# Optimization experiments

Hardware: AMD Instinct MI355X
Metric: run time of the kernel (lower is better)

Reference implementation:

```python
import jax, jax.numpy as jnp
import numpy as np

N = 50000       # nodes
E = 1600000     # edges (before self-loops)
H = 4           # heads
C = 32          # channels per head
G = 64          # graphs in batch
NEG_SLOPE = 0.2


def gat_conv(x, src, dst, W, att_src, att_dst, bias):
    # x: [N, Fin]; W: [Fin, H*C]; att_*: [H, C]; bias: [H*C]
    h = (x @ W).reshape(N, H, C)                       # [N, H, C]
    a_src = jnp.einsum('nhc,hc->nh', h, att_src)       # [N, H]
    a_dst = jnp.einsum('nhc,hc->nh', h, att_dst)       # [N, H]
    e = a_src[src] + a_dst[dst]                        # [E', H]
    e = jax.nn.leaky_relu(e, NEG_SLOPE)
    # softmax over incoming edges of each destination node
    m = jax.ops.segment_max(e, dst, num_segments=N)    # [N, H]
    ex = jnp.exp(e - m[dst])
    denom = jax.ops.segment_sum(ex, dst, num_segments=N)  # [N, H]
    alpha = ex / (denom[dst] + 1e-16)                  # [E', H]
    msg = h[src] * alpha[:, :, None]                   # [E', H, C]
    out = jax.ops.segment_sum(msg, dst, num_segments=N)  # [N, H, C]
    return out.reshape(N, H * C) + bias


def setup_inputs() -> dict:
    key = jax.random.key(0)
    ks = jax.random.split(key, 12)
    x = jax.random.normal(ks[0], (N, 128), dtype=jnp.float32)
    edge_index = jax.random.randint(ks[1], (2, E), 0, N, dtype=jnp.int64)
    batch = jnp.sort(jax.random.randint(ks[2], (N,), 0, G, dtype=jnp.int64))
    s = 0.05
    return {
        'x': x,
        'edge_index': edge_index,
        'batch': batch,
        'W1': jax.random.normal(ks[3], (128, H * C), dtype=jnp.float32) * s,
        'att_src1': jax.random.normal(ks[4], (H, C), dtype=jnp.float32) * s,
        'att_dst1': jax.random.normal(ks[5], (H, C), dtype=jnp.float32) * s,
        'b1': jnp.zeros((H * C,), dtype=jnp.float32),
        'W2': jax.random.normal(ks[6], (H * C, H * C), dtype=jnp.float32) * s,
        'att_src2': jax.random.normal(ks[7], (H, C), dtype=jnp.float32) * s,
        'att_dst2': jax.random.normal(ks[8], (H, C), dtype=jnp.float32) * s,
        'b2': jnp.zeros((H * C,), dtype=jnp.float32),
        'fc_W': jax.random.normal(ks[9], (H * C, 8), dtype=jnp.float32) * s,
        'fc_b': jnp.zeros((8,), dtype=jnp.float32),
    }


def reference(x, edge_index, batch, W1, att_src1, att_dst1, b1,
              W2, att_src2, att_dst2, b2, fc_W, fc_b):
    # add self loops (PyG GATConv default)
    ar = jnp.arange(N, dtype=edge_index.dtype)
    src = jnp.concatenate([edge_index[0], ar])
    dst = jnp.concatenate([edge_index[1], ar])
    h = gat_conv(x, src, dst, W1, att_src1, att_dst1, b1)
    h = jax.nn.elu(h)
    h = gat_conv(h, src, dst, W2, att_src2, att_dst2, b2)
    # global mean pool over graphs
    sums = jax.ops.segment_sum(h, batch, num_segments=G)          # [G, HC]
    cnt = jax.ops.segment_sum(jnp.ones((N,), h.dtype), batch, num_segments=G)
    pooled = sums / jnp.maximum(cnt, 1.0)[:, None]
    logits = pooled @ fc_W + fc_b                                  # [G, 8]
    return jax.nn.log_softmax(logits, axis=1)
```

## Files before the change

kernel.cpp:

```cpp
#include <hip/hip_runtime.h>
#include <math.h>

#define HC 128
#define GG 64
#define NEG 0.2f
#define TILE 8192
#define BW 128
#define SLOT 8192
#define NBMAX 512
#define LDA 136
#define PPARTS 8

typedef __attribute__((ext_vector_type(8))) short short8;
typedef __attribute__((ext_vector_type(4))) float floatx4;
typedef __attribute__((ext_vector_type(2))) float floatx2;

static __device__ __forceinline__ float leaky(float x) { return x > 0.f ? x : NEG * x; }

static __device__ __forceinline__ unsigned short f2bf(float f) {
    unsigned u = __float_as_uint(f);
    u += 0x7FFF + ((u >> 16) & 1);
    return (unsigned short)(u >> 16);
}
static __device__ __forceinline__ float bf2f(unsigned short s) {
    return __uint_as_float(((unsigned)s) << 16);
}

#if __has_builtin(__builtin_amdgcn_cvt_pk_f32_fp8) && __has_builtin(__builtin_amdgcn_cvt_pk_fp8_f32)
template <bool HI>
static __device__ __forceinline__ floatx2 fp8pair(unsigned int w) {
    return __builtin_amdgcn_cvt_pk_f32_fp8((int)w, HI);
}
static __device__ __forceinline__ unsigned int f32x2_fp8(float a, float b) {
    return ((unsigned int)__builtin_amdgcn_cvt_pk_fp8_f32(a, b, 0, false)) & 0xFFFFu;
}
#else
static __device__ __forceinline__ float fp8one(unsigned v) {
    unsigned e = (v >> 3) & 15u, m = v & 7u;
    float mag = e ? __uint_as_float(((e + 120u) << 23) | (m << 20))
                  : (float)m * 0.001953125f;
    return (v & 0x80u) ? -mag : mag;
}
template <bool HI>
static __device__ __forceinline__ floatx2 fp8pair(unsigned int w) {
    unsigned h = HI ? (w >> 16) : w;
    floatx2 r; r.x = fp8one(h & 0xFFu); r.y = fp8one((h >> 8) & 0xFFu);
    return r;
}
static __device__ __forceinline__ unsigned fp8enc(float f) {
    unsigned u = __float_as_uint(f);
    unsigned s = (u >> 24) & 0x80u;
    float a = fabsf(f);
    if (a >= 448.f) return s | 0x7Eu;
    if (a < 0.015625f) {
        unsigned m = (unsigned)(int)rintf(a * 512.f);
        return s | m;
    }
    u = __float_as_uint(a);
    u += 0xFFFFFu + ((u >> 20) & 1u);
    unsigned e8 = (u >> 23) - 120u;
    if (e8 >= 16u) return s | 0x7Eu;
    return s | (e8 << 3) | ((u >> 20) & 7u);
}
static __device__ __forceinline__ unsigned int f32x2_fp8(float a, float b) {
    return fp8enc(a) | (fp8enc(b) << 8);
}
#endif

static __device__ __forceinline__ void acc16(floatx2* acc, float w, const uint4& d) {
    floatx2 w2 = {w, w};
    acc[0] += w2 * fp8pair<false>(d.x);
    acc[1] += w2 * fp8pair<true>(d.x);
    acc[2] += w2 * fp8pair<false>(d.y);
    acc[3] += w2 * fp8pair<true>(d.y);
    acc[4] += w2 * fp8pair<false>(d.z);
    acc[5] += w2 * fp8pair<true>(d.z);
    acc[6] += w2 * fp8pair<false>(d.w);
    acc[7] += w2 * fp8pair<true>(d.w);
}

__global__ __launch_bounds__(256) void setup_k(const float* __restrict__ W1,
                                               const float* __restrict__ W2,
                                               unsigned short* __restrict__ Wt1,
                                               unsigned short* __restrict__ Wt2,
                                               int* __restrict__ gbcur,
                                               const int* __restrict__ batch,
                                               int* __restrict__ node_end,
                                               int* __restrict__ row_start,
                                               int NB, int Nn, int M) {
    int i = blockIdx.x * 256 + threadIdx.x;
    if (i < NB) gbcur[i] = i * SLOT;
    if (i == 0) row_start[Nn] = M;
    if (i < 32768) {
        const float* W = (i >> 14) ? W2 : W1;
        unsigned short* Wt = (i >> 14) ? Wt2 : Wt1;
        int d = i & 16383;
        int j = d & 7;
        int m = (d >> 3) & 15;
        int qf = d >> 7;
        int q = qf & 3;
        int f = qf >> 2;
        int kb = f & 3;
        int ct = f >> 2;
        int n = ct * 16 + m;
        int k = kb * 32 + q * 8 + j;
        Wt[d] = f2bf(W[k * 128 + n]);
    }
    if (i < Nn) {
        int b = batch[i];
        if (i == 0) {
            for (int g = 0; g < b; g++) node_end[g] = 0;
        }
        int bn = (i + 1 < Nn) ? batch[i + 1] : GG;
        for (int g = b; g < bn; g++) node_end[g] = i + 1;
    }
}

__global__ __launch_bounds__(256) void binscat_k(const int* __restrict__ ei,
                                                 int* __restrict__ gbcur,
                                                 unsigned int* __restrict__ staging,
                                                 int E, int M, int NB) {
    __shared__ unsigned int reorder[TILE];
    __shared__ int s_cnt[NBMAX], s_off[NBMAX], s_run[NBMAX];
    __shared__ int s_wsum[8];
    __shared__ int s_carry;
    const int tid = threadIdx.x;
    const int lane = tid & 63, wid = tid >> 6;
    const int tbase = blockIdx.x * TILE;
    const int tcnt = min(TILE, M - tbase);

    for (int i = tid; i < NB; i += 256) s_cnt[i] = 0;
    if (tid == 0) s_carry = 0;
    __syncthreads();

    for (int t = tid; t < tcnt; t += 256) {
        int i = tbase + t;
        int dst = (i < E) ? ei[E + i] : (i - E);
        atomicAdd(&s_cnt[dst >> 7], 1);
    }
    __syncthreads();

    for (int base = 0; base < NB; base += 256) {
        int i = base + tid;
        int v = (i < NB) ? s_cnt[i] : 0;
        int incl = v;
        #pragma unroll
        for (int off = 1; off < 64; off <<= 1) {
            int u = __shfl_up(incl, off);
            if (lane >= off) incl += u;
        }
        if (lane == 63) s_wsum[wid] = incl;
        __syncthreads();
        if (tid == 0) {
            int a = 0;
            for (int w = 0; w < 4; w++) { int tv = s_wsum[w]; s_wsum[w] = a; a += tv; }
            s_wsum[4] = a;
        }
        __syncthreads();
        int excl = s_carry + s_wsum[wid] + incl - v;
        if (i < NB) s_off[i] = excl;
        __syncthreads();
        if (tid == 0) s_carry += s_wsum[4];
        __syncthreads();
    }

    for (int b = tid; b < NB; b += 256)
        s_run[b] = atomicAdd(&gbcur[b], s_cnt[b]);
    for (int b = tid; b < NB; b += 256) s_cnt[b] = s_off[b];
    __syncthreads();

    for (int t = tid; t < tcnt; t += 256) {
        int i = tbase + t;
        int src, dst;
        if (i < E) { src = ei[i]; dst = ei[E + i]; }
        else       { src = dst = i - E; }
        unsigned int p = ((unsigned int)dst << 16) | (unsigned int)src;
        int r = atomicAdd(&s_cnt[dst >> 7], 1);
        reorder[r] = p;
    }
    __syncthreads();

    for (int t = tid; t < tcnt; t += 256) {
        unsigned int p = reorder[t];
        int b = p >> 23;
        staging[s_run[b] + (t - s_off[b])] = p;
    }
}

__global__ __launch_bounds__(256) void unbin_k(const unsigned int* __restrict__ staging,
                                               const int* __restrict__ gbcur,
                                               int* __restrict__ row_start,
                                               unsigned short* __restrict__ srcs, int Nn) {
    __shared__ int s_cnt[BW];
    __shared__ int s_cur[BW];
    __shared__ int s_w[4];
    int b = blockIdx.x, t = threadIdx.x;
    int sbase = b * SLOT;
    int cnt = gbcur[b] - sbase;

    int pacc = 0;
    for (int i = t; i < b; i += 256) pacc += gbcur[i] - i * SLOT;
    #pragma unroll
    for (int off = 1; off < 64; off <<= 1) pacc += __shfl_xor(pacc, off);
    if ((t & 63) == 0) s_w[t >> 6] = pacc;
    __syncthreads();
    int bb = s_w[0] + s_w[1] + s_w[2] + s_w[3];
    __syncthreads();

    int n0 = b * BW;
    if (t < BW) s_cnt[t] = 0;
    __syncthreads();
    for (int j = t; j < cnt; j += 256)
        atomicAdd(&s_cnt[(staging[sbase + j] >> 16) & (BW - 1)], 1);
    __syncthreads();
    int v = (t < BW) ? s_cnt[t] : 0;
    int incl = v;
    #pragma unroll
    for (int off = 1; off < 64; off <<= 1) {
        int u = __shfl_up(incl, off);
        if ((t & 63) >= off) incl += u;
    }
    if (t < BW && (t & 63) == 63) s_w[t >> 6] = incl;
    __syncthreads();
    int excl = incl - v + ((t >= 64 && t < BW) ? s_w[0] : 0);
    if (t < BW) {
        s_cur[t] = bb + excl;
        if (n0 + t < Nn) row_start[n0 + t] = bb + excl;
    }
    __syncthreads();
    for (int j = t; j < cnt; j += 256) {
        unsigned int p = staging[sbase + j];
        int ln = (int)(p >> 16) & (BW - 1);
        int r = atomicAdd(&s_cur[ln], 1);
        srcs[r] = (unsigned short)(p & 0xFFFFu);
    }
}

__global__ __launch_bounds__(128) void gemm_fused(const void* __restrict__ Xv,
                                                  int x_f32,
                                                  const unsigned short* __restrict__ Wt,
                                                  const float* __restrict__ att_s,
                                                  const float* __restrict__ att_d,
                                                  unsigned char* __restrict__ H8,
                                                  float* __restrict__ a_src,
                                                  float* __restrict__ a_dst,
                                                  int n_rows) {
    __shared__ unsigned short As[64 * LDA];
    const int tid = threadIdx.x;
    const int row0 = blockIdx.x * 64;

    if (x_f32) {
        const float* X = (const float*)Xv;
        for (int i = tid; i < 2048; i += 128) {
            int r = i >> 5;
            int c4 = (i & 31) << 2;
            int gr = row0 + r;
            float4 v = (gr < n_rows) ? ((const float4*)&X[(size_t)gr * 128])[i & 31]
                                     : make_float4(0.f, 0.f, 0.f, 0.f);
            ushort4 bv = {f2bf(v.x), f2bf(v.y), f2bf(v.z), f2bf(v.w)};
            *(ushort4*)&As[r * LDA + c4] = bv;
        }
    } else {
        const unsigned short* X = (const unsigned short*)Xv;
        for (int i = tid; i < 1024; i += 128) {
            int r = i >> 4;
            int c8 = (i & 15) << 3;
            int gr = row0 + r;
            uint4 v = (gr < n_rows) ? *(const uint4*)&X[(size_t)gr * 128 + c8]
                                    : make_uint4(0, 0, 0, 0);
            *(uint4*)&As[r * LDA + c8] = v;
        }
    }
    __syncthreads();

    const int lane = tid & 63;
    const int wave = tid >> 6;
    const int m = lane & 15;
    const int quad = lane >> 4;
    const int wr0 = wave * 32;

    floatx4 acc[2][8];
    #pragma unroll
    for (int nt = 0; nt < 2; nt++)
        #pragma unroll
        for (int ct = 0; ct < 8; ct++)
            acc[nt][ct] = (floatx4){0.f, 0.f, 0.f, 0.f};

    #pragma unroll
    for (int kb = 0; kb < 4; kb++) {
        short8 x0 = *(const short8*)&As[(wr0 + m) * LDA + kb * 32 + quad * 8];
        short8 x1 = *(const short8*)&As[(wr0 + 16 + m) * LDA + kb * 32 + quad * 8];
        #pragma unroll
        for (int ct = 0; ct < 8; ct++) {
            short8 wf = *(const short8*)&Wt[(((ct * 4 + kb) * 4) + quad) * 128 + m * 8];
            acc[0][ct] = __builtin_amdgcn_mfma_f32_16x16x32_bf16(wf, x0, acc[0][ct], 0, 0, 0);
            acc[1][ct] = __builtin_amdgcn_mfma_f32_16x16x32_bf16(wf, x1, acc[1][ct], 0, 0, 0);
        }
    }

    const int q4 = quad * 4;
    #pragma unroll
    for (int nt = 0; nt < 2; nt++) {
        int node = row0 + wr0 + nt * 16 + m;
        bool vld = node < n_rows;
        float ps[4] = {0.f, 0.f, 0.f, 0.f};
        float pd[4] = {0.f, 0.f, 0.f, 0.f};
        #pragma unroll
        for (int ct = 0; ct < 8; ct++) {
            floatx4 v = acc[nt][ct];
            int c0 = ct * 16 + q4;
            float4 avs = *(const float4*)&att_s[c0];
            float4 avd = *(const float4*)&att_d[c0];
            int h = ct >> 1;
            ps[h] += v[0] * avs.x + v[1] * avs.y + v[2] * avs.z + v[3] * avs.w;
            pd[h] += v[0] * avd.x + v[1] * avd.y + v[2] * avd.z + v[3] * avd.w;
            if (vld) {
                unsigned pk01 = f32x2_fp8(v[0], v[1]);
                unsigned pk23 = f32x2_fp8(v[2], v[3]);
                *(unsigned*)&H8[(size_t)node * 128 + c0] = pk01 | (pk23 << 16);
            }
        }
        #pragma unroll
        for (int h = 0; h < 4; h++) {
            ps[h] += __shfl_xor(ps[h], 16); ps[h] += __shfl_xor(ps[h], 32);
            pd[h] += __shfl_xor(pd[h], 16); pd[h] += __shfl_xor(pd[h], 32);
        }
        if (lane < 16 && vld) {
            float4 s4 = {ps[0], ps[1], ps[2], ps[3]};
            float4 d4 = {pd[0], pd[1], pd[2], pd[3]};
            *(float4*)&a_src[node * 4] = s4;
            *(float4*)&a_dst[node * 4] = d4;
        }
    }
}

__global__ __launch_bounds__(256) void gat_agg(const unsigned char* __restrict__ H8,
                                               const float* __restrict__ a_src,
                                               const float* __restrict__ a_dst,
                                               const int* __restrict__ row_start,
                                               const unsigned short* __restrict__ srcs,
                                               const float* __restrict__ bias,
                                               unsigned short* __restrict__ OUT,
                                               int n_rows, int elu) {
    int n = (blockIdx.x * 256 + threadIdx.x) >> 3;
    if (n >= n_rows) return;
    int li = threadIdx.x & 7;
    int hd = li >> 1;
    int base = row_start[n];
    int end = row_start[n + 1];
    float adh = a_dst[n * 4 + hd];

    floatx2 acc[8];
    #pragma unroll
    for (int k = 0; k < 8; k++) acc[k] = (floatx2){0.f, 0.f};
    float wsum = 0.f;

    int j = base;
    int head_n = min(end - j, (4 - (base & 3)) & 3);
    for (int q = 0; q < head_n; q++, j++) {
        int s0 = srcs[j];
        float w0 = __expf(leaky(a_src[s0 * 4 + hd] + adh));
        uint4 d0 = *(const uint4*)&H8[(size_t)s0 * 128 + li * 16];
        acc16(acc, w0, d0);
        wsum += w0;
    }
    for (; j + 4 <= end; j += 4) {
        uint2 sv = *(const uint2*)&srcs[j];
        int s0 = sv.x & 0xFFFFu, s1 = sv.x >> 16;
        int s2 = sv.y & 0xFFFFu, s3 = sv.y >> 16;
        float a0 = a_src[s0 * 4 + hd];
        float a1 = a_src[s1 * 4 + hd];
        float a2 = a_src[s2 * 4 + hd];
        float a3 = a_src[s3 * 4 + hd];
        uint4 d0 = *(const uint4*)&H8[(size_t)s0 * 128 + li * 16];
        uint4 d1 = *(const uint4*)&H8[(size_t)s1 * 128 + li * 16];
        uint4 d2 = *(const uint4*)&H8[(size_t)s2 * 128 + li * 16];
        uint4 d3 = *(const uint4*)&H8[(size_t)s3 * 128 + li * 16];
        float w0 = __expf(leaky(a0 + adh));
        float w1 = __expf(leaky(a1 + adh));
        float w2 = __expf(leaky(a2 + adh));
        float w3 = __expf(leaky(a3 + adh));
        acc16(acc, w0, d0);
        acc16(acc, w1, d1);
        acc16(acc, w2, d2);
        acc16(acc, w3, d3);
        wsum += (w0 + w1) + (w2 + w3);
    }
    for (; j < end; j++) {
        int s0 = srcs[j];
        float w0 = __expf(leaky(a_src[s0 * 4 + hd] + adh));
        uint4 d0 = *(const uint4*)&H8[(size_t)s0 * 128 + li * 16];
        acc16(acc, w0, d0);
        wsum += w0;
    }

    float ih = 1.0f / (wsum + 1e-16f);
    float o[16];
    #pragma unroll
    for (int k = 0; k < 8; k++) {
        float2 bv = *(const float2*)&bias[li * 16 + 2 * k];
        o[2 * k]     = acc[k].x * ih + bv.x;
        o[2 * k + 1] = acc[k].y * ih + bv.y;
    }
    if (elu) {
        #pragma unroll
        for (int k = 0; k < 16; k++) o[k] = o[k] > 0.f ? o[k] : __expf(o[k]) - 1.f;
    }
    unsigned int pk[8];
    #pragma unroll
    for (int k = 0; k < 8; k++)
        pk[k] = ((unsigned)f2bf(o[2 * k + 1]) << 16) | (unsigned)f2bf(o[2 * k]);
    uint4 s0v = {pk[0], pk[1], pk[2], pk[3]};
    uint4 s1v = {pk[4], pk[5], pk[6], pk[7]};
    unsigned short* op = &OUT[(size_t)n * 128 + li * 16];
    *(uint4*)op = s0v;
    *(uint4*)(op + 8) = s1v;
}

__global__ __launch_bounds__(256) void pool_k(const unsigned* __restrict__ H2u,
                                              const int* __restrict__ node_end,
                                              float* __restrict__ partial) {
    __shared__ float ls[4][128];
    int g = blockIdx.x >> 3;
    int p = blockIdx.x & (PPARTS - 1);
    int s = (g > 0) ? node_end[g - 1] : 0;
    int e = node_end[g];
    int cnt = e - s;
    int chunk = (cnt + PPARTS - 1) >> 3;
    int n0 = s + p * chunk;
    int n1 = min(n0 + chunk, e);
    int col = threadIdx.x & 63;
    int nr = threadIdx.x >> 6;
    float ax = 0.f, ay = 0.f;
    for (int n = n0 + nr; n < n1; n += 4) {
        unsigned u = H2u[(size_t)n * 64 + col];
        ax += bf2f((unsigned short)(u & 0xFFFFu));
        ay += bf2f((unsigned short)(u >> 16));
    }
    ls[nr][col * 2] = ax;
    ls[nr][col * 2 + 1] = ay;
    __syncthreads();
    if (threadIdx.x < 128) {
        float v = ls[0][threadIdx.x] + ls[1][threadIdx.x] +
                  ls[2][threadIdx.x] + ls[3][threadIdx.x];
        partial[(size_t)(p * GG + g) * 128 + threadIdx.x] = v;
    }
}

__global__ __launch_bounds__(64) void head_k(const float* __restrict__ partial,
                                             const int* __restrict__ node_end,
                                             const float* __restrict__ fcW,
                                             const float* __restrict__ fcb,
                                             float* __restrict__ out) {
    __shared__ float p[128];
    __shared__ float lg[8];
    int g = blockIdx.x, t = threadIdx.x;
    int c = node_end[g] - (g > 0 ? node_end[g - 1] : 0);
    float cnt = fmaxf((float)c, 1.0f);
    float v0 = 0.f, v1 = 0.f;
    #pragma unroll
    for (int q = 0; q < PPARTS; q++) {
        v0 += partial[(size_t)(q * GG + g) * 128 + t];
        v1 += partial[(size_t)(q * GG + g) * 128 + 64 + t];
    }
    p[t] = v0 / cnt;
    p[t + 64] = v1 / cnt;
    __syncthreads();
    if (t < 8) {
        float s = fcb[t];
        for (int k = 0; k < 128; k++) s += p[k] * fcW[k * 8 + t];
        lg[t] = s;
    }
    __syncthreads();
    if (t == 0) {
        float m = lg[0];
        for (int j = 1; j < 8; j++) m = fmaxf(m, lg[j]);
        float se = 0.f;
        for (int j = 0; j < 8; j++) se += expf(lg[j] - m);
        float lse = logf(se) + m;
        for (int j = 0; j < 8; j++) out[g * 8 + j] = lg[j] - lse;
    }
}

extern "C" void kernel_launch(void* const* d_in, const int* in_sizes, int n_in,
                              void* d_out, int out_size, void* d_ws, size_t ws_size,
                              hipStream_t stream) {
    const float* x    = (const float*)d_in[0];
    const int*   ei   = (const int*)d_in[1];
    const int*   batch= (const int*)d_in[2];
    const float* W1   = (const float*)d_in[3];
    const float* as1  = (const float*)d_in[4];
    const float* ad1  = (const float*)d_in[5];
    const float* b1   = (const float*)d_in[6];
    const float* W2   = (const float*)d_in[7];
    const float* as2  = (const float*)d_in[8];
    const float* ad2  = (const float*)d_in[9];
    const float* b2   = (const float*)d_in[10];
    const float* fcW  = (const float*)d_in[11];
    const float* fcb  = (const float*)d_in[12];
    float* out = (float*)d_out;

    const int Nn = in_sizes[0] / HC;
    const int E  = in_sizes[1] / 2;
    const int M  = E + Nn;
    const int NB = (Nn + BW - 1) / BW;

    char* ws = (char*)d_ws;
    size_t off = 0;
    auto alloc = [&](size_t bytes) -> char* {
        char* p = ws + off;
        off = (off + bytes + 255) & ~(size_t)255;
        return p;
    };
    size_t hB_bytes  = (size_t)Nn * HC * 2;
    size_t stg_bytes = (size_t)NB * SLOT * 4;
    char* hB_region = alloc(hB_bytes > stg_bytes ? hB_bytes : stg_bytes);
    unsigned short* hB      = (unsigned short*)hB_region;
    unsigned int*   staging = (unsigned int*)hB_region;
    unsigned char*  H8      = (unsigned char*)alloc((size_t)Nn * HC);
    float* asrc      = (float*)alloc((size_t)Nn * 4 * 4);
    float* adst      = (float*)alloc((size_t)Nn * 4 * 4);
    unsigned short* srcs = (unsigned short*)alloc((size_t)M * 2);
    int*   row_start = (int*)alloc((size_t)(Nn + 1) * 4);
    float* partial   = (float*)alloc((size_t)PPARTS * GG * HC * 4);
    int*   node_end  = (int*)alloc((size_t)GG * 4);
    int*   gbcur     = (int*)alloc((size_t)NB * 4);
    unsigned short* Wt1 = (unsigned short*)alloc(16384 * 2);
    unsigned short* Wt2 = (unsigned short*)alloc(16384 * 2);

    setup_k<<<(Nn + 255) / 256, 256, 0, stream>>>(W1, W2, Wt1, Wt2, gbcur, batch,
                                                  node_end, row_start, NB, Nn, M);
    binscat_k<<<(M + TILE - 1) / TILE, 256, 0, stream>>>(ei, gbcur, staging, E, M, NB);
    unbin_k<<<NB, 256, 0, stream>>>(staging, gbcur, row_start, srcs, Nn);
    gemm_fused<<<(Nn + 63) / 64, 128, 0, stream>>>(x, 1, Wt1, as1, ad1, H8, asrc, adst, Nn);
    gat_agg<<<(Nn + 31) / 32, 256, 0, stream>>>(H8, asrc, adst, row_start, srcs, b1, hB, Nn, 1);
    gemm_fused<<<(Nn + 63) / 64, 128, 0, stream>>>(hB, 0, Wt2, as2, ad2, H8, asrc, adst, Nn);
    gat_agg<<<(Nn + 31) / 32, 256, 0, stream>>>(H8, asrc, adst, row_start, srcs, b2, hB, Nn, 0);
    pool_k<<<GG * PPARTS, 256, 0, stream>>>((const unsigned*)hB, node_end, partial);
    head_k<<<GG, 64, 0, stream>>>(partial, node_end, fcW, fcb, out);
}
```

Measured before the change: 262.5 us.

## Merge edge binning with layer-1 GEMM and fuse mean pooling into aggregation

Edge binning and the first-layer GEMM now run in one launch, with blocks split by index between the two roles, so the independent GEMM overlaps the binning work. The second aggregation writes per-block, per-graph partial sums straight from shared memory instead of writing hB and running a separate pooling kernel. The head kernel sums those block partials for each graph. This removes two launches and one full pass over the layer-2 output. The pooling assumes each 32-node block covers at most 4 graphs (it relies on sorted batch), and the layer-1 GEMM now uses 16 rows per wave.

```diff
diff --git a/kernel.cpp b/kernel.cpp
--- a/kernel.cpp
+++ b/kernel.cpp
@@ -9,7 +9,6 @@
 #define SLOT 8192
 #define NBMAX 512
 #define LDA 136
-#define PPARTS 8
 
 typedef __attribute__((ext_vector_type(8))) short short8;
 typedef __attribute__((ext_vector_type(4))) float floatx4;
@@ -116,74 +115,155 @@
     }
 }
 
-__global__ __launch_bounds__(256) void binscat_k(const int* __restrict__ ei,
-                                                 int* __restrict__ gbcur,
-                                                 unsigned int* __restrict__ staging,
-                                                 int E, int M, int NB) {
-    __shared__ unsigned int reorder[TILE];
-    __shared__ int s_cnt[NBMAX], s_off[NBMAX], s_run[NBMAX];
-    __shared__ int s_wsum[8];
-    __shared__ int s_carry;
+__global__ __launch_bounds__(256) void fused_k(const int* __restrict__ ei,
+                                               int* __restrict__ gbcur,
+                                               unsigned int* __restrict__ staging,
+                                               int E, int M, int NB, int NBIN,
+                                               const float* __restrict__ X,
+                                               const unsigned short* __restrict__ Wt,
+                                               const float* __restrict__ att_s,
+                                               const float* __restrict__ att_d,
+                                               unsigned char* __restrict__ H8,
+                                               float* __restrict__ a_src,
+                                               float* __restrict__ a_dst,
+                                               int n_rows) {
+    __shared__ __align__(16) char smem[39040];
     const int tid = threadIdx.x;
-    const int lane = tid & 63, wid = tid >> 6;
-    const int tbase = blockIdx.x * TILE;
-    const int tcnt = min(TILE, M - tbase);
-
-    for (int i = tid; i < NB; i += 256) s_cnt[i] = 0;
-    if (tid == 0) s_carry = 0;
-    __syncthreads();
-
-    for (int t = tid; t < tcnt; t += 256) {
-        int i = tbase + t;
-        int dst = (i < E) ? ei[E + i] : (i - E);
-        atomicAdd(&s_cnt[dst >> 7], 1);
-    }
-    __syncthreads();
-
-    for (int base = 0; base < NB; base += 256) {
-        int i = base + tid;
-        int v = (i < NB) ? s_cnt[i] : 0;
-        int incl = v;
-        #pragma unroll
-        for (int off = 1; off < 64; off <<= 1) {
-            int u = __shfl_up(incl, off);
-            if (lane >= off) incl += u;
-        }
-        if (lane == 63) s_wsum[wid] = incl;
+
+    if ((int)blockIdx.x < NBIN) {
+        unsigned int* reorder = (unsigned int*)smem;
+        int* s_cnt  = (int*)(smem + 32768);
+        int* s_off  = (int*)(smem + 34816);
+        int* s_run  = (int*)(smem + 36864);
+        int* s_wsum = (int*)(smem + 38912);
+        int* s_carry= (int*)(smem + 38944);
+        const int lane = tid & 63, wid = tid >> 6;
+        const int tbase = blockIdx.x * TILE;
+        const int tcnt = min(TILE, M - tbase);
+
+        for (int i = tid; i < NB; i += 256) s_cnt[i] = 0;
+        if (tid == 0) *s_carry = 0;
         __syncthreads();
-        if (tid == 0) {
-            int a = 0;
-            for (int w = 0; w < 4; w++) { int tv = s_wsum[w]; s_wsum[w] = a; a += tv; }
-            s_wsum[4] = a;
+
+        for (int t = tid; t < tcnt; t += 256) {
+            int i = tbase + t;
+            int dst = (i < E) ? ei[E + i] : (i - E);
+            atomicAdd(&s_cnt[dst >> 7], 1);
         }
         __syncthreads();
-        int excl = s_carry + s_wsum[wid] + incl - v;
-        if (i < NB) s_off[i] = excl;
+
+        for (int base = 0; base < NB; base += 256) {
+            int i = base + tid;
+            int v = (i < NB) ? s_cnt[i] : 0;
+            int incl = v;
+            #pragma unroll
+            for (int off = 1; off < 64; off <<= 1) {
+                int u = __shfl_up(incl, off);
+                if (lane >= off) incl += u;
+            }
+            if (lane == 63) s_wsum[wid] = incl;
+            __syncthreads();
+            if (tid == 0) {
+                int a = 0;
+                for (int w = 0; w < 4; w++) { int tv = s_wsum[w]; s_wsum[w] = a; a += tv; }
+                s_wsum[4] = a;
+            }
+            __syncthreads();
+            int excl = *s_carry + s_wsum[wid] + incl - v;
+            if (i < NB) s_off[i] = excl;
+            __syncthreads();
+            if (tid == 0) *s_carry += s_wsum[4];
+            __syncthreads();
+        }
+
+        for (int b = tid; b < NB; b += 256)
+            s_run[b] = atomicAdd(&gbcur[b], s_cnt[b]);
+        for (int b = tid; b < NB; b += 256) s_cnt[b] = s_off[b];
         __syncthreads();
-        if (tid == 0) s_carry += s_wsum[4];
+
+        for (int t = tid; t < tcnt; t += 256) {
+            int i = tbase + t;
+            int src, dst;
+            if (i < E) { src = ei[i]; dst = ei[E + i]; }
+            else       { src = dst = i - E; }
+            unsigned int p = ((unsigned int)dst << 16) | (unsigned int)src;
+            int r = atomicAdd(&s_cnt[dst >> 7], 1);
+            reorder[r] = p;
+        }
         __syncthreads();
-    }
-
-    for (int b = tid; b < NB; b += 256)
-        s_run[b] = atomicAdd(&gbcur[b], s_cnt[b]);
-    for (int b = tid; b < NB; b += 256) s_cnt[b] = s_off[b];
-    __syncthreads();
-
-    for (int t = tid; t < tcnt; t += 256) {
-        int i = tbase + t;
-        int src, dst;
-        if (i < E) { src = ei[i]; dst = ei[E + i]; }
-        else       { src = dst = i - E; }
-        unsigned int p = ((unsigned int)dst << 16) | (unsigned int)src;
-        int r = atomicAdd(&s_cnt[dst >> 7], 1);
-        reorder[r] = p;
-    }
-    __syncthreads();
-
-    for (int t = tid; t < tcnt; t += 256) {
-        unsigned int p = reorder[t];
-        int b = p >> 23;
-        staging[s_run[b] + (t - s_off[b])] = p;
+
+        for (int t = tid; t < tcnt; t += 256) {
+            unsigned int p = reorder[t];
+            int b = p >> 23;
+            staging[s_run[b] + (t - s_off[b])] = p;
+        }
+    } else {
+        unsigned short* As = (unsigned short*)smem;
+        const int gb = blockIdx.x - NBIN;
+        const int row0 = gb * 64;
+
+        for (int i = tid; i < 2048; i += 256) {
+            int r = i >> 5;
+            int c4 = (i & 31) << 2;
+            int gr = row0 + r;
+            float4 v = (gr < n_rows) ? ((const float4*)&X[(size_t)gr * 128])[i & 31]
+                                     : make_float4(0.f, 0.f, 0.f, 0.f);
+            ushort4 bv = {f2bf(v.x), f2bf(v.y), f2bf(v.z), f2bf(v.w)};
+            *(ushort4*)&As[r * LDA + c4] = bv;
+        }
+        __syncthreads();
+
+        const int lane = tid & 63;
+        const int wave = tid >> 6;
+        const int m = lane & 15;
+        const int quad = lane >> 4;
+        const int wr = wave * 16;
+
+        floatx4 acc[8];
+        #pragma unroll
+        for (int ct = 0; ct < 8; ct++) acc[ct] = (floatx4){0.f, 0.f, 0.f, 0.f};
+
+        #pragma unroll
+        for (int kb = 0; kb < 4; kb++) {
+            short8 x0 = *(const short8*)&As[(wr + m) * LDA + kb * 32 + quad * 8];
+            #pragma unroll
+            for (int ct = 0; ct < 8; ct++) {
+                short8 wf = *(const short8*)&Wt[(((ct * 4 + kb) * 4) + quad) * 128 + m * 8];
+                acc[ct] = __builtin_amdgcn_mfma_f32_16x16x32_bf16(wf, x0, acc[ct], 0, 0, 0);
+            }
+        }
+
+        const int q4 = quad * 4;
+        int node = row0 + wr + m;
+        bool vld = node < n_rows;
+        float ps[4] = {0.f, 0.f, 0.f, 0.f};
+        float pd[4] = {0.f, 0.f, 0.f, 0.f};
+        #pragma unroll
+        for (int ct = 0; ct < 8; ct++) {
+            floatx4 v = acc[ct];
+            int c0 = ct * 16 + q4;
+            float4 avs = *(const float4*)&att_s[c0];
+            float4 avd = *(const float4*)&att_d[c0];
+            int h = ct >> 1;
+            ps[h] += v[0] * avs.x + v[1] * avs.y + v[2] * avs.z + v[3] * avs.w;
+            pd[h] += v[0] * avd.x + v[1] * avd.y + v[2] * avd.z + v[3] * avd.w;
+            if (vld) {
+                unsigned pk01 = f32x2_fp8(v[0], v[1]);
+                unsigned pk23 = f32x2_fp8(v[2], v[3]);
+                *(unsigned*)&H8[(size_t)node * 128 + c0] = pk01 | (pk23 << 16);
+            }
+        }
+        #pragma unroll
+        for (int h = 0; h < 4; h++) {
+            ps[h] += __shfl_xor(ps[h], 16); ps[h] += __shfl_xor(ps[h], 32);
+            pd[h] += __shfl_xor(pd[h], 16); pd[h] += __shfl_xor(pd[h], 32);
+        }
+        if (lane < 16 && vld) {
+            float4 s4 = {ps[0], ps[1], ps[2], ps[3]};
+            float4 d4 = {pd[0], pd[1], pd[2], pd[3]};
+            *(float4*)&a_src[node * 4] = s4;
+            *(float4*)&a_dst[node * 4] = d4;
+        }
     }
 }
 
@@ -236,8 +316,7 @@
     }
 }
 
-__global__ __launch_bounds__(128) void gemm_fused(const void* __restrict__ Xv,
-                                                  int x_f32,
+__global__ __launch_bounds__(128) void gemm_fused(const unsigned short* __restrict__ X,
                                                   const unsigned short* __restrict__ Wt,
                                                   const float* __restrict__ att_s,
                                                   const float* __restrict__ att_d,
@@ -249,27 +328,13 @@
     const int tid = threadIdx.x;
     const int row0 = blockIdx.x * 64;
 
-    if (x_f32) {
-        const float* X = (const float*)Xv;
-        for (int i = tid; i < 2048; i += 128) {
-            int r = i >> 5;
-            int c4 = (i & 31) << 2;
-            int gr = row0 + r;
-            float4 v = (gr < n_rows) ? ((const float4*)&X[(size_t)gr * 128])[i & 31]
-                                     : make_float4(0.f, 0.f, 0.f, 0.f);
-            ushort4 bv = {f2bf(v.x), f2bf(v.y), f2bf(v.z), f2bf(v.w)};
-            *(ushort4*)&As[r * LDA + c4] = bv;
-        }
-    } else {
-        const unsigned short* X = (const unsigned short*)Xv;
-        for (int i = tid; i < 1024; i += 128) {
-            int r = i >> 4;
-            int c8 = (i & 15) << 3;
-            int gr = row0 + r;
-            uint4 v = (gr < n_rows) ? *(const uint4*)&X[(size_t)gr * 128 + c8]
-                                    : make_uint4(0, 0, 0, 0);
-            *(uint4*)&As[r * LDA + c8] = v;
-        }
+    for (int i = tid; i < 1024; i += 128) {
+        int r = i >> 4;
+        int c8 = (i & 15) << 3;
+        int gr = row0 + r;
+        uint4 v = (gr < n_rows) ? *(const uint4*)&X[(size_t)gr * 128 + c8]
+                                : make_uint4(0, 0, 0, 0);
+        *(uint4*)&As[r * LDA + c8] = v;
     }
     __syncthreads();
 
@@ -341,135 +406,154 @@
                                                const unsigned short* __restrict__ srcs,
                                                const float* __restrict__ bias,
                                                unsigned short* __restrict__ OUT,
-                                               int n_rows, int elu) {
+                                               const int* __restrict__ batch,
+                                               float* __restrict__ partial,
+                                               int n_rows, int mode) {
+    __shared__ float ls[32][128];
+    __shared__ int sg[32];
     int n = (blockIdx.x * 256 + threadIdx.x) >> 3;
-    if (n >= n_rows) return;
     int li = threadIdx.x & 7;
     int hd = li >> 1;
-    int base = row_start[n];
-    int end = row_start[n + 1];
-    float adh = a_dst[n * 4 + hd];
-
-    floatx2 acc[8];
-    #pragma unroll
-    for (int k = 0; k < 8; k++) acc[k] = (floatx2){0.f, 0.f};
-    float wsum = 0.f;
-
-    int j = base;
-    int head_n = min(end - j, (4 - (base & 3)) & 3);
-    for (int q = 0; q < head_n; q++, j++) {
-        int s0 = srcs[j];
-        float w0 = __expf(leaky(a_src[s0 * 4 + hd] + adh));
-        uint4 d0 = *(const uint4*)&H8[(size_t)s0 * 128 + li * 16];
-        acc16(acc, w0, d0);
-        wsum += w0;
-    }
-    for (; j + 4 <= end; j += 4) {
-        uint2 sv = *(const uint2*)&srcs[j];
-        int s0 = sv.x & 0xFFFFu, s1 = sv.x >> 16;
-        int s2 = sv.y & 0xFFFFu, s3 = sv.y >> 16;
-        float a0 = a_src[s0 * 4 + hd];
-        float a1 = a_src[s1 * 4 + hd];
-        float a2 = a_src[s2 * 4 + hd];
-        float a3 = a_src[s3 * 4 + hd];
-        uint4 d0 = *(const uint4*)&H8[(size_t)s0 * 128 + li * 16];
-        uint4 d1 = *(const uint4*)&H8[(size_t)s1 * 128 + li * 16];
-        uint4 d2 = *(const uint4*)&H8[(size_t)s2 * 128 + li * 16];
-        uint4 d3 = *(const uint4*)&H8[(size_t)s3 * 128 + li * 16];
-        float w0 = __expf(leaky(a0 + adh));
-        float w1 = __expf(leaky(a1 + adh));
-        float w2 = __expf(leaky(a2 + adh));
-        float w3 = __expf(leaky(a3 + adh));
-        acc16(acc, w0, d0);
-        acc16(acc, w1, d1);
-        acc16(acc, w2, d2);
-        acc16(acc, w3, d3);
-        wsum += (w0 + w1) + (w2 + w3);
-    }
-    for (; j < end; j++) {
-        int s0 = srcs[j];
-        float w0 = __expf(leaky(a_src[s0 * 4 + hd] + adh));
-        uint4 d0 = *(const uint4*)&H8[(size_t)s0 * 128 + li * 16];
-        acc16(acc, w0, d0);
-        wsum += w0;
-    }
-
-    float ih = 1.0f / (wsum + 1e-16f);
+    bool vld = n < n_rows;
+
     float o[16];
     #pragma unroll
-    for (int k = 0; k < 8; k++) {
-        float2 bv = *(const float2*)&bias[li * 16 + 2 * k];
-        o[2 * k]     = acc[k].x * ih + bv.x;
-        o[2 * k + 1] = acc[k].y * ih + bv.y;
-    }
-    if (elu) {
-        #pragma unroll
-        for (int k = 0; k < 16; k++) o[k] = o[k] > 0.f ? o[k] : __expf(o[k]) - 1.f;
-    }
-    unsigned int pk[8];
-    #pragma unroll
-    for (int k = 0; k < 8; k++)
-        pk[k] = ((unsigned)f2bf(o[2 * k + 1]) << 16) | (unsigned)f2bf(o[2 * k]);
-    uint4 s0v = {pk[0], pk[1], pk[2], pk[3]};
-    uint4 s1v = {pk[4], pk[5], pk[6], pk[7]};
-    unsigned short* op = &OUT[(size_t)n * 128 + li * 16];
-    *(uint4*)op = s0v;
-    *(uint4*)(op + 8) = s1v;
-}
-
-__global__ __launch_bounds__(256) void pool_k(const unsigned* __restrict__ H2u,
-                                              const int* __restrict__ node_end,
-                                              float* __restrict__ partial) {
-    __shared__ float ls[4][128];
-    int g = blockIdx.x >> 3;
-    int p = blockIdx.x & (PPARTS - 1);
-    int s = (g > 0) ? node_end[g - 1] : 0;
-    int e = node_end[g];
-    int cnt = e - s;
-    int chunk = (cnt + PPARTS - 1) >> 3;
-    int n0 = s + p * chunk;
-    int n1 = min(n0 + chunk, e);
-    int col = threadIdx.x & 63;
-    int nr = threadIdx.x >> 6;
-    float ax = 0.f, ay = 0.f;
-    for (int n = n0 + nr; n < n1; n += 4) {
-        unsigned u = H2u[(size_t)n * 64 + col];
-        ax += bf2f((unsigned short)(u & 0xFFFFu));
-        ay += bf2f((unsigned short)(u >> 16));
-    }
-    ls[nr][col * 2] = ax;
-    ls[nr][col * 2 + 1] = ay;
-    __syncthreads();
-    if (threadIdx.x < 128) {
-        float v = ls[0][threadIdx.x] + ls[1][threadIdx.x] +
-                  ls[2][threadIdx.x] + ls[3][threadIdx.x];
-        partial[(size_t)(p * GG + g) * 128 + threadIdx.x] = v;
+    for (int k = 0; k < 16; k++) o[k] = 0.f;
+
+    if (vld) {
+        int base = row_start[n];
+        int end = row_start[n + 1];
+        float adh = a_dst[n * 4 + hd];
+
+        floatx2 acc[8];
+        #pragma unroll
+        for (int k = 0; k < 8; k++) acc[k] = (floatx2){0.f, 0.f};
+        float wsum = 0.f;
+
+        int j = base;
+        int head_n = min(end - j, (4 - (base & 3)) & 3);
+        for (int q = 0; q < head_n; q++, j++) {
+            int s0 = srcs[j];
+            float w0 = __expf(leaky(a_src[s0 * 4 + hd] + adh));
+            uint4 d0 = *(const uint4*)&H8[(size_t)s0 * 128 + li * 16];
+            acc16(acc, w0, d0);
+            wsum += w0;
+        }
+        for (; j + 4 <= end; j += 4) {
+            uint2 sv = *(const uint2*)&srcs[j];
+            int s0 = sv.x & 0xFFFFu, s1 = sv.x >> 16;
+            int s2 = sv.y & 0xFFFFu, s3 = sv.y >> 16;
+            float a0 = a_src[s0 * 4 + hd];
+            float a1 = a_src[s1 * 4 + hd];
+            float a2 = a_src[s2 * 4 + hd];
+            float a3 = a_src[s3 * 4 + hd];
+            uint4 d0 = *(const uint4*)&H8[(size_t)s0 * 128 + li * 16];
+            uint4 d1 = *(const uint4*)&H8[(size_t)s1 * 128 + li * 16];
+            uint4 d2 = *(const uint4*)&H8[(size_t)s2 * 128 + li * 16];
+            uint4 d3 = *(const uint4*)&H8[(size_t)s3 * 128 + li * 16];
+            float w0 = __expf(leaky(a0 + adh));
+            float w1 = __expf(leaky(a1 + adh));
+            float w2 = __expf(leaky(a2 + adh));
+            float w3 = __expf(leaky(a3 + adh));
+            acc16(acc, w0, d0);
+            acc16(acc, w1, d1);
+            acc16(acc, w2, d2);
+            acc16(acc, w3, d3);
+            wsum += (w0 + w1) + (w2 + w3);
+        }
+        for (; j < end; j++) {
+            int s0 = srcs[j];
+            float w0 = __expf(leaky(a_src[s0 * 4 + hd] + adh));
+            uint4 d0 = *(const uint4*)&H8[(size_t)s0 * 128 + li * 16];
+            acc16(acc, w0, d0);
+            wsum += w0;
+        }
+
+        float ih = 1.0f / (wsum + 1e-16f);
+        #pragma unroll
+        for (int k = 0; k < 8; k++) {
+            float2 bv = *(const float2*)&bias[li * 16 + 2 * k];
+            o[2 * k]     = acc[k].x * ih + bv.x;
+            o[2 * k + 1] = acc[k].y * ih + bv.y;
+        }
+    }
+
+    if (mode == 0) {
+        if (vld) {
+            #pragma unroll
+            for (int k = 0; k < 16; k++) o[k] = o[k] > 0.f ? o[k] : __expf(o[k]) - 1.f;
+            unsigned int pk[8];
+            #pragma unroll
+            for (int k = 0; k < 8; k++)
+                pk[k] = ((unsigned)f2bf(o[2 * k + 1]) << 16) | (unsigned)f2bf(o[2 * k]);
+            uint4 s0v = {pk[0], pk[1], pk[2], pk[3]};
+            uint4 s1v = {pk[4], pk[5], pk[6], pk[7]};
+            unsigned short* op = &OUT[(size_t)n * 128 + li * 16];
+            *(uint4*)op = s0v;
+            *(uint4*)(op + 8) = s1v;
+        }
+    } else {
+        int nl = threadIdx.x >> 3;
+        int n0b = blockIdx.x * 32;
+        float* row = &ls[nl][li * 16];
+        *(float4*)&row[0]  = (float4){o[0], o[1], o[2], o[3]};
+        *(float4*)&row[4]  = (float4){o[4], o[5], o[6], o[7]};
+        *(float4*)&row[8]  = (float4){o[8], o[9], o[10], o[11]};
+        *(float4*)&row[12] = (float4){o[12], o[13], o[14], o[15]};
+        if (li == 0) sg[nl] = vld ? min(batch[n] - batch[n0b], 3) : 0;
+        __syncthreads();
+        int t = threadIdx.x;
+        if (t < 128) {
+            float a0 = 0.f, a1 = 0.f, a2 = 0.f, a3 = 0.f;
+            #pragma unroll 8
+            for (int r = 0; r < 32; r++) {
+                float v = ls[r][t];
+                int gr = sg[r];
+                a0 += (gr == 0) ? v : 0.f;
+                a1 += (gr == 1) ? v : 0.f;
+                a2 += (gr == 2) ? v : 0.f;
+                a3 += (gr == 3) ? v : 0.f;
+            }
+            float* pp = &partial[(size_t)blockIdx.x * 4 * 128];
+            pp[t] = a0;
+            pp[128 + t] = a1;
+            pp[256 + t] = a2;
+            pp[384 + t] = a3;
+        }
     }
 }
 
 __global__ __launch_bounds__(64) void head_k(const float* __restrict__ partial,
                                              const int* __restrict__ node_end,
+                                             const int* __restrict__ batch,
                                              const float* __restrict__ fcW,
                                              const float* __restrict__ fcb,
-                                             float* __restrict__ out) {
+                                             float* __restrict__ out, int n_rows) {
     __shared__ float p[128];
     __shared__ float lg[8];
     int g = blockIdx.x, t = threadIdx.x;
-    int c = node_end[g] - (g > 0 ? node_end[g - 1] : 0);
-    float cnt = fmaxf((float)c, 1.0f);
+    int s = (g > 0) ? node_end[g - 1] : 0;
+    int e = node_end[g];
+    float cnt = fmaxf((float)(e - s), 1.0f);
     float v0 = 0.f, v1 = 0.f;
-    #pragma unroll
-    for (int q = 0; q < PPARTS; q++) {
-        v0 += partial[(size_t)(q * GG + g) * 128 + t];
-        v1 += partial[(size_t)(q * GG + g) * 128 + 64 + t];
+    if (e > s) {
+        int b0 = s >> 5;
+        int b1 = (e - 1) >> 5;
+        for (int b = b0; b <= b1; b++) {
+            int slot = g - batch[b * 32];
+            if (slot < 0 || slot > 3) continue;
+            const float* pp = &partial[((size_t)b * 4 + slot) * 128];
+            v0 += pp[t];
+            v1 += pp[64 + t];
+        }
     }
     p[t] = v0 / cnt;
     p[t + 64] = v1 / cnt;
     __syncthreads();
     if (t < 8) {
-        float s = fcb[t];
-        for (int k = 0; k < 128; k++) s += p[k] * fcW[k * 8 + t];
-        lg[t] = s;
+        float sacc = fcb[t];
+        for (int k = 0; k < 128; k++) sacc += p[k] * fcW[k * 8 + t];
+        lg[t] = sacc;
     }
     __syncthreads();
     if (t == 0) {
@@ -504,6 +588,9 @@
     const int E  = in_sizes[1] / 2;
     const int M  = E + Nn;
     const int NB = (Nn + BW - 1) / BW;
+    const int NBIN = (M + TILE - 1) / TILE;
+    const int GB1 = (Nn + 63) / 64;
+    const int NBLK2 = (Nn + 31) / 32;
 
     char* ws = (char*)d_ws;
     size_t off = 0;
@@ -522,7 +609,7 @@
     float* adst      = (float*)alloc((size_t)Nn * 4 * 4);
     unsigned short* srcs = (unsigned short*)alloc((size_t)M * 2);
     int*   row_start = (int*)alloc((size_t)(Nn + 1) * 4);
-    float* partial   = (float*)alloc((size_t)PPARTS * GG * HC * 4);
+    float* partial   = (float*)alloc((size_t)NBLK2 * 4 * HC * 4);
     int*   node_end  = (int*)alloc((size_t)GG * 4);
     int*   gbcur     = (int*)alloc((size_t)NB * 4);
     unsigned short* Wt1 = (unsigned short*)alloc(16384 * 2);
@@ -530,12 +617,13 @@
 
     setup_k<<<(Nn + 255) / 256, 256, 0, stream>>>(W1, W2, Wt1, Wt2, gbcur, batch,
                                                   node_end, row_start, NB, Nn, M);
-    binscat_k<<<(M + TILE - 1) / TILE, 256, 0, stream>>>(ei, gbcur, staging, E, M, NB);
+    fused_k<<<NBIN + GB1, 256, 0, stream>>>(ei, gbcur, staging, E, M, NB, NBIN,
+                                            x, Wt1, as1, ad1, H8, asrc, adst, Nn);
     unbin_k<<<NB, 256, 0, stream>>>(staging, gbcur, row_start, srcs, Nn);
-    gemm_fused<<<(Nn + 63) / 64, 128, 0, stream>>>(x, 1, Wt1, as1, ad1, H8, asrc, adst, Nn);
-    gat_agg<<<(Nn + 31) / 32, 256, 0, stream>>>(H8, asrc, adst, row_start, srcs, b1, hB, Nn, 1);
-    gemm_fused<<<(Nn + 63) / 64, 128, 0, stream>>>(hB, 0, Wt2, as2, ad2, H8, asrc, adst, Nn);
-    gat_agg<<<(Nn + 31) / 32, 256, 0, stream>>>(H8, asrc, adst, row_start, srcs, b2, hB, Nn, 0);
-    pool_k<<<GG * PPARTS, 256, 0, stream>>>((const unsigned*)hB, node_end, partial);
-    head_k<<<GG, 64, 0, stream>>>(partial, node_end, fcW, fcb, out);
-}
+    gat_agg<<<NBLK2, 256, 0, stream>>>(H8, asrc, adst, row_start, srcs, b1, hB,
+                                       batch, partial, Nn, 0);
+    gemm_fused<<<GB1, 128, 0, stream>>>(hB, Wt2, as2, ad2, H8, asrc, adst, Nn);
+    gat_agg<<<NBLK2, 256, 0, stream>>>(H8, asrc, adst, row_start, srcs, b2, hB,
+                                       batch, partial, Nn, 1);
+    head_k<<<GG, 64, 0, stream>>>(partial, node_end, batch, fcW, fcb, out, Nn);
+}
```

Result: faster. 244.8 us (-6.7%).
